# Optimization experiments

Measured on AMD Instinct MI355X. Metric: run time of the kernel, lower is better.

## Reference

```python
import jax, jax.numpy as jnp
import numpy as np

B, OBS, NH, LAT = 8192, 256, 2048, 128

def setup_inputs() -> dict:
    key = jax.random.key(0)
    k1, k2, k3, k4, k5, k6 = jax.random.split(key, 6)
    s1 = 1.0 / np.sqrt(OBS + NH)
    s2 = 1.0 / np.sqrt(NH)
    return {
        "x": jax.random.normal(k1, (B, OBS), dtype=jnp.float32),
        "h": jax.random.normal(k2, (B, NH), dtype=jnp.float32),
        "W_i2h": jax.random.normal(k3, (NH, OBS + NH), dtype=jnp.float32) * s1,
        "b_i2h": jax.random.normal(k4, (NH,), dtype=jnp.float32) * s1,
        "W_h2o": jax.random.normal(k5, (2 * LAT, NH), dtype=jnp.float32) * s2,
        "b_h2o": jax.random.normal(k6, (2 * LAT,), dtype=jnp.float32) * s2,
    }

def reference(x, h, W_i2h, b_i2h, W_h2o, b_h2o):
    # combined = cat((x, h), dim=1)  -> [B, OBS+NH]
    combined = jnp.concatenate([x, h], axis=1)
    # h_new = tanh(i2h(combined));  Linear is y = x @ W.T + b
    h_new = jnp.tanh(combined @ W_i2h.T + b_i2h)
    out = h_new @ W_h2o.T + b_h2o  # [B, 2*LAT]
    return (out, h_new)
```

## Files before the change

### kernel.cpp

```cpp
#include <hip/hip_runtime.h>
#include <hip/hip_bf16.h>
#include <cstdint>

using bf16 = __hip_bfloat16;
typedef __attribute__((ext_vector_type(8))) short short8;
typedef __attribute__((ext_vector_type(4))) float floatx4;

static constexpr int BATCH = 8192;
static constexpr int K1    = 2304;
static constexpr int N1    = 2048;
static constexpr int K2    = 2048;
static constexpr int N2    = 256;
static constexpr int KT1   = K1 / 64;

__device__ __forceinline__ void gload_lds16(const void* g, void* l) {
  __builtin_amdgcn_global_load_lds(
      (const __attribute__((address_space(1))) void*)g,
      (__attribute__((address_space(3))) void*)l, 16, 0, 0);
}

__device__ __forceinline__ float fast_tanh(float x) {
  float e = __builtin_amdgcn_exp2f(x * 2.8853900817779268f);
  return 1.0f - 2.0f * __builtin_amdgcn_rcpf(e + 1.0f);
}

__device__ __forceinline__ short8 cvt8(const float* src) {
  float4 a = ((const float4*)src)[0];
  float4 b = ((const float4*)src)[1];
  union { short8 v; bf16 e[8]; } u;
  u.e[0] = __float2bfloat16(a.x); u.e[1] = __float2bfloat16(a.y);
  u.e[2] = __float2bfloat16(a.z); u.e[3] = __float2bfloat16(a.w);
  u.e[4] = __float2bfloat16(b.x); u.e[5] = __float2bfloat16(b.y);
  u.e[6] = __float2bfloat16(b.z); u.e[7] = __float2bfloat16(b.w);
  return u.v;
}

static constexpr int SEG0 = BATCH * (K1 / 8);
static constexpr int SEG1 = N1 * K1 / 8;
static constexpr int SEG2 = N2 * K2 / 8;
__global__ __launch_bounds__(256) void prep(
    const float* __restrict__ x, const float* __restrict__ h,
    const float* __restrict__ W1, const float* __restrict__ W2,
    bf16* __restrict__ comb, bf16* __restrict__ W1b, bf16* __restrict__ W2b) {
  int i = blockIdx.x * 256 + threadIdx.x;
  if (i < SEG0) {
    int row  = i / 288;
    int slot = i - row * 288;
    const float* src = (slot < 32) ? (x + (size_t)row * 256 + slot * 8)
                                   : (h + (size_t)row * 2048 + (slot - 32) * 8);
    *(short8*)(comb + (size_t)row * 2304 + slot * 8) = cvt8(src);
  } else if (i < SEG0 + SEG1) {
    int j = i - SEG0;
    *(short8*)(W1b + (size_t)j * 8) = cvt8(W1 + (size_t)j * 8);
  } else {
    int j = i - (SEG0 + SEG1);
    *(short8*)(W2b + (size_t)j * 8) = cvt8(W2 + (size_t)j * 8);
  }
}

__global__ __launch_bounds__(256) void bias_init(
    const float* __restrict__ bias, float* __restrict__ out) {
  int i = blockIdx.x * 256 + threadIdx.x;
  float4 b = ((const float4*)bias)[i & 63];
  ((float4*)out)[i] = b;
}

__global__ __launch_bounds__(512, 2) void gemm1_tanh(
    const bf16* __restrict__ A, const bf16* __restrict__ W,
    const float* __restrict__ bias,
    float* __restrict__ hf32, bf16* __restrict__ hb16) {
  __shared__ bf16 lds[2][2][2][8192];
  const int t    = threadIdx.x;
  const int lane = t & 63;
  const int wave = t >> 6;
  const int wm   = (wave >> 2) * 128;
  const int wn   = (wave & 3) * 64;
  const int quad = lane >> 4;
  const int r15  = lane & 15;

  const int srow  = t >> 2;
  const int sslot = t & 3;
  const int sq    = (sslot ^ (srow & 3)) * 8;

  const size_t Abase = (size_t)blockIdx.x * 256 * K1;
  const size_t Bbase = (size_t)blockIdx.y * 256 * K1;
  const size_t gA0 = Abase + (size_t)srow * K1 + sq;
  const size_t gA1 = Abase + (size_t)(srow + 128) * K1 + sq;
  const size_t gB0 = Bbase + (size_t)srow * K1 + sq;
  const size_t gB1 = Bbase + (size_t)(srow + 128) * K1 + sq;
  const int d0 = t * 16, d1 = 8192 + t * 16;

#define STAGE(sb, mat_, skh, skt) do {                                       \
    const int ktc_ = ((skt) < KT1 ? (skt) : (KT1 - 1));                      \
    const size_t ko_ = (size_t)ktc_ * 64 + (skh) * 32;                       \
    const bf16* p0_ = (mat_) ? (W + gB0 + ko_) : (A + gA0 + ko_);            \
    const bf16* p1_ = (mat_) ? (W + gB1 + ko_) : (A + gA1 + ko_);            \
    gload_lds16(p0_, (char*)&lds[sb][mat_][skh][0] + d0);                    \
    gload_lds16(p1_, (char*)&lds[sb][mat_][skh][0] + d1);                    \
  } while (0)

  floatx4 acc[8][4];
  const floatx4 z = {0.f, 0.f, 0.f, 0.f};
#pragma unroll
  for (int i = 0; i < 8; i++)
#pragma unroll
    for (int j = 0; j < 4; j++) acc[i][j] = z;

  STAGE(0, 0, 0, 0); STAGE(0, 1, 0, 0); STAGE(0, 0, 1, 0); STAGE(0, 1, 1, 0);
  STAGE(1, 0, 0, 1); STAGE(1, 1, 0, 1);
  asm volatile("s_waitcnt vmcnt(4)" ::: "memory");
  __builtin_amdgcn_s_barrier();

#define PHASE(cb, ks, mtg, sb, smat, skh, skt, VMW) do {                     \
    short8 af_[4], bf_[4];                                                   \
    _Pragma("unroll")                                                        \
    for (int mt = 0; mt < 4; ++mt) {                                         \
      const int row = wm + (mtg) * 64 + mt * 16 + r15;                       \
      af_[mt] = *(const short8*)((const char*)&lds[cb][0][ks][0] +           \
                                 row * 64 + ((quad ^ (row & 3)) << 4));      \
    }                                                                        \
    _Pragma("unroll")                                                        \
    for (int nt = 0; nt < 4; ++nt) {                                         \
      const int row = wn + nt * 16 + r15;                                    \
      bf_[nt] = *(const short8*)((const char*)&lds[cb][1][ks][0] +           \
                                 row * 64 + ((quad ^ (row & 3)) << 4));      \
    }                                                                        \
    STAGE(sb, smat, skh, skt);                                               \
    __builtin_amdgcn_sched_barrier(0);                                       \
    if (VMW) asm volatile("s_waitcnt vmcnt(4)" ::: "memory");                \
    __builtin_amdgcn_s_barrier();                                            \
    asm volatile("s_waitcnt lgkmcnt(0)" ::: "memory");                       \
    __builtin_amdgcn_sched_barrier(0);                                       \
    __builtin_amdgcn_s_setprio(1);                                           \
    _Pragma("unroll")                                                        \
    for (int mt = 0; mt < 4; ++mt)                                           \
      _Pragma("unroll")                                                      \
      for (int nt = 0; nt < 4; ++nt)                                         \
        acc[(mtg) * 4 + mt][nt] = __builtin_amdgcn_mfma_f32_16x16x32_bf16(   \
            af_[mt], bf_[nt], acc[(mtg) * 4 + mt][nt], 0, 0, 0);             \
    __builtin_amdgcn_s_setprio(0);                                           \
    __builtin_amdgcn_s_barrier();                                            \
  } while (0)

#pragma clang loop unroll(disable)
  for (int t2 = 0; t2 < KT1 / 2; ++t2) {
    const int n = 2 * t2;
    PHASE(0, 0, 0,  1, 0, 1, n + 1, 0);
    PHASE(0, 0, 1,  1, 1, 1, n + 1, 0);
    PHASE(0, 1, 0,  0, 0, 0, n + 2, 0);
    PHASE(0, 1, 1,  0, 1, 0, n + 2, 1);
    PHASE(1, 0, 0,  0, 0, 1, n + 2, 0);
    PHASE(1, 0, 1,  0, 1, 1, n + 2, 0);
    PHASE(1, 1, 0,  1, 0, 0, n + 3, 0);
    PHASE(1, 1, 1,  1, 1, 0, n + 3, 1);
  }
#undef PHASE
#undef STAGE

  const int gcol0 = blockIdx.y * 256 + wn;
  float bv[4];
#pragma unroll
  for (int nt = 0; nt < 4; ++nt) bv[nt] = bias[gcol0 + nt * 16 + r15];
  const size_t grow0 = (size_t)blockIdx.x * 256 + wm;
#pragma unroll
  for (int mt = 0; mt < 8; ++mt) {
#pragma unroll
    for (int i = 0; i < 4; ++i) {
      const size_t gr = grow0 + mt * 16 + quad * 4 + i;
      const size_t rb = gr * (size_t)N1;
#pragma unroll
      for (int nt = 0; nt < 4; ++nt) {
        const int gc = gcol0 + nt * 16 + r15;
        float v = fast_tanh(acc[mt][nt][i] + bv[nt]);
        hf32[rb + gc] = v;
        hb16[rb + gc] = __float2bfloat16(v);
      }
    }
  }
}

__global__ __launch_bounds__(256) void gemm2_out(
    const bf16* __restrict__ A, const bf16* __restrict__ W,
    float* __restrict__ out) {
  __shared__ bf16 As[32 * 64];
  __shared__ bf16 Bs[256 * 64];
  const int t    = threadIdx.x;
  const int lane = t & 63;
  const int wave = t >> 6;
  const int quad = lane >> 4;
  const int r15  = lane & 15;
  const int srow = t >> 3;
  const int sc   = t & 7;

  const int mrow0 = blockIdx.x * 32;
  const int kbase = blockIdx.y * (K2 / 2);

  floatx4 acc[2][4];
  const floatx4 z = {0.f, 0.f, 0.f, 0.f};
#pragma unroll
  for (int i = 0; i < 2; i++)
#pragma unroll
    for (int j = 0; j < 4; j++) acc[i][j] = z;

  for (int kt = 0; kt < 16; ++kt) {
    const int k0 = kbase + kt * 64;
    __syncthreads();
    {
      int row = srow;
      int gc  = k0 + ((sc ^ (row & 7)) << 3);
      gload_lds16(A + (size_t)(mrow0 + row) * K2 + gc, (char*)As + t * 16);
    }
#pragma unroll
    for (int it = 0; it < 8; ++it) {
      int row = it * 32 + srow;
      int gc  = k0 + ((sc ^ (row & 7)) << 3);
      gload_lds16(W + (size_t)row * K2 + gc,
                  (char*)Bs + it * 4096 + t * 16);
    }
    __syncthreads();
#pragma unroll
    for (int ks = 0; ks < 2; ++ks) {
      short8 af[2], bfr[4];
      const int kq = ks * 4 + quad;
#pragma unroll
      for (int mt = 0; mt < 2; ++mt) {
        int row = mt * 16 + r15;
        af[mt] = *(const short8*)((const char*)As + row * 128 +
                                  ((kq ^ (row & 7)) << 4));
      }
#pragma unroll
      for (int nt = 0; nt < 4; ++nt) {
        int row = wave * 64 + nt * 16 + r15;
        bfr[nt] = *(const short8*)((const char*)Bs + row * 128 +
                                   ((kq ^ (row & 7)) << 4));
      }
#pragma unroll
      for (int mt = 0; mt < 2; ++mt)
#pragma unroll
        for (int nt = 0; nt < 4; ++nt)
          acc[mt][nt] = __builtin_amdgcn_mfma_f32_16x16x32_bf16(
              af[mt], bfr[nt], acc[mt][nt], 0, 0, 0);
    }
  }

  const int gcol0 = wave * 64;
#pragma unroll
  for (int mt = 0; mt < 2; ++mt) {
#pragma unroll
    for (int i = 0; i < 4; ++i) {
      size_t gr = (size_t)mrow0 + mt * 16 + quad * 4 + i;
      size_t rb = gr * (size_t)N2;
#pragma unroll
      for (int nt = 0; nt < 4; ++nt) {
        int gc = gcol0 + nt * 16 + r15;
        unsafeAtomicAdd(&out[rb + gc], acc[mt][nt][i]);
      }
    }
  }
}

extern "C" void kernel_launch(void* const* d_in, const int* in_sizes, int n_in,
                              void* d_out, int out_size, void* d_ws,
                              size_t ws_size, hipStream_t stream) {
  const float* x     = (const float*)d_in[0];
  const float* h     = (const float*)d_in[1];
  const float* W_i2h = (const float*)d_in[2];
  const float* b_i2h = (const float*)d_in[3];
  const float* W_h2o = (const float*)d_in[4];
  const float* b_h2o = (const float*)d_in[5];

  float* out       = (float*)d_out;
  float* hnew_f32  = out + (size_t)BATCH * N2;

  bf16* comb   = (bf16*)d_ws;
  bf16* Wi2h_b = comb + (size_t)BATCH * K1;
  bf16* Wh2o_b = Wi2h_b + (size_t)N1 * K1;
  bf16* hnew_b = Wh2o_b + (size_t)N2 * K2;

  bias_init<<<(BATCH * N2 / 4) / 256, 256, 0, stream>>>(b_h2o, out);

  prep<<<(SEG0 + SEG1 + SEG2) / 256, 256, 0, stream>>>(
      x, h, W_i2h, W_h2o, comb, Wi2h_b, Wh2o_b);

  gemm1_tanh<<<dim3(BATCH / 256, N1 / 256), 512, 0, stream>>>(
      comb, Wi2h_b, b_i2h, hnew_f32, hnew_b);

  gemm2_out<<<dim3(BATCH / 32, 2), 256, 0, stream>>>(hnew_b, Wh2o_b, out);
}
```

Before: 266.7 us.

## Merge bias init into prep, restructure gemm1 phases, double-buffer gemm2

```diff
diff --git a/kernel.cpp b/kernel.cpp
--- a/kernel.cpp
+++ b/kernel.cpp
@@ -38,10 +38,13 @@
 static constexpr int SEG0 = BATCH * (K1 / 8);
 static constexpr int SEG1 = N1 * K1 / 8;
 static constexpr int SEG2 = N2 * K2 / 8;
+static constexpr int SEG3 = BATCH * (N2 / 4);
 __global__ __launch_bounds__(256) void prep(
     const float* __restrict__ x, const float* __restrict__ h,
     const float* __restrict__ W1, const float* __restrict__ W2,
-    bf16* __restrict__ comb, bf16* __restrict__ W1b, bf16* __restrict__ W2b) {
+    const float* __restrict__ b2,
+    bf16* __restrict__ comb, bf16* __restrict__ W1b, bf16* __restrict__ W2b,
+    float* __restrict__ outp) {
   int i = blockIdx.x * 256 + threadIdx.x;
   if (i < SEG0) {
     int row  = i / 288;
@@ -52,17 +55,14 @@
   } else if (i < SEG0 + SEG1) {
     int j = i - SEG0;
     *(short8*)(W1b + (size_t)j * 8) = cvt8(W1 + (size_t)j * 8);
-  } else {
+  } else if (i < SEG0 + SEG1 + SEG2) {
     int j = i - (SEG0 + SEG1);
     *(short8*)(W2b + (size_t)j * 8) = cvt8(W2 + (size_t)j * 8);
-  }
-}
-
-__global__ __launch_bounds__(256) void bias_init(
-    const float* __restrict__ bias, float* __restrict__ out) {
-  int i = blockIdx.x * 256 + threadIdx.x;
-  float4 b = ((const float4*)bias)[i & 63];
-  ((float4*)out)[i] = b;
+  } else {
+    int j = i - (SEG0 + SEG1 + SEG2);
+    float4 b = ((const float4*)b2)[j & 63];
+    ((float4*)outp)[j] = b;
+  }
 }
 
 __global__ __launch_bounds__(512, 2) void gemm1_tanh(
@@ -78,9 +78,13 @@
   const int quad = lane >> 4;
   const int r15  = lane & 15;
 
+  const int swz   = ((quad ^ ((r15 >> 1) & 3)) << 4);
+  const int baseA = wm * 64 + r15 * 64 + swz;
+  const int baseB = 32768 + wn * 64 + r15 * 64 + swz;
+
   const int srow  = t >> 2;
   const int sslot = t & 3;
-  const int sq    = (sslot ^ (srow & 3)) * 8;
+  const int sq    = (sslot ^ ((srow >> 1) & 3)) * 8;
 
   const size_t Abase = (size_t)blockIdx.x * 256 * K1;
   const size_t Bbase = (size_t)blockIdx.y * 256 * K1;
@@ -89,14 +93,16 @@
   const size_t gB0 = Bbase + (size_t)srow * K1 + sq;
   const size_t gB1 = Bbase + (size_t)(srow + 128) * K1 + sq;
   const int d0 = t * 16, d1 = 8192 + t * 16;
-
-#define STAGE(sb, mat_, skh, skt) do {                                       \
+  char* const ldsb = (char*)lds;
+
+#define STAGE2(sb, skh, skt) do {                                            \
     const int ktc_ = ((skt) < KT1 ? (skt) : (KT1 - 1));                      \
     const size_t ko_ = (size_t)ktc_ * 64 + (skh) * 32;                       \
-    const bf16* p0_ = (mat_) ? (W + gB0 + ko_) : (A + gA0 + ko_);            \
-    const bf16* p1_ = (mat_) ? (W + gB1 + ko_) : (A + gA1 + ko_);            \
-    gload_lds16(p0_, (char*)&lds[sb][mat_][skh][0] + d0);                    \
-    gload_lds16(p1_, (char*)&lds[sb][mat_][skh][0] + d1);                    \
+    char* const la_ = ldsb + ((sb) << 16) + ((skh) << 14);                   \
+    gload_lds16(A + gA0 + ko_, la_ + d0);                                    \
+    gload_lds16(A + gA1 + ko_, la_ + d1);                                    \
+    gload_lds16(W + gB0 + ko_, la_ + 32768 + d0);                            \
+    gload_lds16(W + gB1 + ko_, la_ + 32768 + d1);                            \
   } while (0)
 
   floatx4 acc[8][4];
@@ -106,38 +112,48 @@
 #pragma unroll
     for (int j = 0; j < 4; j++) acc[i][j] = z;
 
-  STAGE(0, 0, 0, 0); STAGE(0, 1, 0, 0); STAGE(0, 0, 1, 0); STAGE(0, 1, 1, 0);
-  STAGE(1, 0, 0, 1); STAGE(1, 1, 0, 1);
+  STAGE2(0, 0, 0); STAGE2(0, 1, 0); STAGE2(1, 0, 1);
   asm volatile("s_waitcnt vmcnt(4)" ::: "memory");
   __builtin_amdgcn_s_barrier();
 
-#define PHASE(cb, ks, mtg, sb, smat, skh, skt, VMW) do {                     \
-    short8 af_[4], bf_[4];                                                   \
-    _Pragma("unroll")                                                        \
-    for (int mt = 0; mt < 4; ++mt) {                                         \
-      const int row = wm + (mtg) * 64 + mt * 16 + r15;                       \
-      af_[mt] = *(const short8*)((const char*)&lds[cb][0][ks][0] +           \
-                                 row * 64 + ((quad ^ (row & 3)) << 4));      \
-    }                                                                        \
-    _Pragma("unroll")                                                        \
-    for (int nt = 0; nt < 4; ++nt) {                                         \
-      const int row = wn + nt * 16 + r15;                                    \
-      bf_[nt] = *(const short8*)((const char*)&lds[cb][1][ks][0] +           \
-                                 row * 64 + ((quad ^ (row & 3)) << 4));      \
-    }                                                                        \
-    STAGE(sb, smat, skh, skt);                                               \
-    __builtin_amdgcn_sched_barrier(0);                                       \
-    if (VMW) asm volatile("s_waitcnt vmcnt(4)" ::: "memory");                \
+#define MPHASE(cb, ks, sb, skh, skt, VMW) do {                               \
+    STAGE2(sb, skh, skt);                                                    \
+    __builtin_amdgcn_sched_barrier(0);                                       \
+    if (VMW) asm volatile("s_waitcnt vmcnt(8)" ::: "memory");                \
     __builtin_amdgcn_s_barrier();                                            \
-    asm volatile("s_waitcnt lgkmcnt(0)" ::: "memory");                       \
+    asm volatile("" ::: "memory");          \
+    const char* Lb_ = ldsb + ((cb) << 16) + ((ks) << 14);                    \
+    short8 bf_[4], af0_[4], af1_[4];                                         \
+    _Pragma("unroll")                                                        \
+    for (int nt = 0; nt < 4; ++nt)                                           \
+      bf_[nt] = *(const short8*)(Lb_ + baseB + nt * 1024);                   \
+    _Pragma("unroll")                                                        \
+    for (int mt = 0; mt < 4; ++mt)                                           \
+      af0_[mt] = *(const short8*)(Lb_ + baseA + mt * 1024);                  \
+    __builtin_amdgcn_sched_barrier(0);                                       \
+    _Pragma("unroll")                                                        \
+    for (int mt = 0; mt < 4; ++mt)                                           \
+      af1_[mt] = *(const short8*)(Lb_ + baseA + 4096 + mt * 1024);           \
+    __builtin_amdgcn_sched_barrier(0);                                       \
+    asm volatile("s_waitcnt lgkmcnt(4)" ::: "memory");                       \
     __builtin_amdgcn_sched_barrier(0);                                       \
     __builtin_amdgcn_s_setprio(1);                                           \
     _Pragma("unroll")                                                        \
     for (int mt = 0; mt < 4; ++mt)                                           \
       _Pragma("unroll")                                                      \
       for (int nt = 0; nt < 4; ++nt)                                         \
-        acc[(mtg) * 4 + mt][nt] = __builtin_amdgcn_mfma_f32_16x16x32_bf16(   \
-            af_[mt], bf_[nt], acc[(mtg) * 4 + mt][nt], 0, 0, 0);             \
+        acc[mt][nt] = __builtin_amdgcn_mfma_f32_16x16x32_bf16(               \
+            af0_[mt], bf_[nt], acc[mt][nt], 0, 0, 0);                        \
+    __builtin_amdgcn_s_setprio(0);                                           \
+    asm volatile("s_waitcnt lgkmcnt(0)" ::: "memory");                       \
+    __builtin_amdgcn_sched_barrier(0);                                       \
+    __builtin_amdgcn_s_setprio(1);                                           \
+    _Pragma("unroll")                                                        \
+    for (int mt = 0; mt < 4; ++mt)                                           \
+      _Pragma("unroll")                                                      \
+      for (int nt = 0; nt < 4; ++nt)                                         \
+        acc[4 + mt][nt] = __builtin_amdgcn_mfma_f32_16x16x32_bf16(           \
+            af1_[mt], bf_[nt], acc[4 + mt][nt], 0, 0, 0);                    \
     __builtin_amdgcn_s_setprio(0);                                           \
     __builtin_amdgcn_s_barrier();                                            \
   } while (0)
@@ -145,17 +161,13 @@
 #pragma clang loop unroll(disable)
   for (int t2 = 0; t2 < KT1 / 2; ++t2) {
     const int n = 2 * t2;
-    PHASE(0, 0, 0,  1, 0, 1, n + 1, 0);
-    PHASE(0, 0, 1,  1, 1, 1, n + 1, 0);
-    PHASE(0, 1, 0,  0, 0, 0, n + 2, 0);
-    PHASE(0, 1, 1,  0, 1, 0, n + 2, 1);
-    PHASE(1, 0, 0,  0, 0, 1, n + 2, 0);
-    PHASE(1, 0, 1,  0, 1, 1, n + 2, 0);
-    PHASE(1, 1, 0,  1, 0, 0, n + 3, 0);
-    PHASE(1, 1, 1,  1, 1, 0, n + 3, 1);
-  }
-#undef PHASE
-#undef STAGE
+    MPHASE(0, 0,  1, 1, n + 1, 0);
+    MPHASE(0, 1,  0, 0, n + 2, 1);
+    MPHASE(1, 0,  0, 1, n + 2, 0);
+    MPHASE(1, 1,  1, 0, n + 3, 1);
+  }
+#undef MPHASE
+#undef STAGE2
 
   const int gcol0 = blockIdx.y * 256 + wn;
   float bv[4];
@@ -182,8 +194,8 @@
 __global__ __launch_bounds__(256) void gemm2_out(
     const bf16* __restrict__ A, const bf16* __restrict__ W,
     float* __restrict__ out) {
-  __shared__ bf16 As[32 * 64];
-  __shared__ bf16 Bs[256 * 64];
+  __shared__ bf16 As[2][32 * 64];
+  __shared__ bf16 Bs[2][256 * 64];
   const int t    = threadIdx.x;
   const int lane = t & 63;
   const int wave = t >> 6;
@@ -195,6 +207,22 @@
   const int mrow0 = blockIdx.x * 32;
   const int kbase = blockIdx.y * (K2 / 2);
 
+#define G2STAGE(b, kt) do {                                                  \
+    const int k0_ = kbase + (kt) * 64;                                       \
+    {                                                                        \
+      int gc_ = k0_ + ((sc ^ (srow & 7)) << 3);                              \
+      gload_lds16(A + (size_t)(mrow0 + srow) * K2 + gc_,                     \
+                  (char*)As[b] + t * 16);                                    \
+    }                                                                        \
+    _Pragma("unroll")                                                        \
+    for (int it = 0; it < 8; ++it) {                                         \
+      int row_ = it * 32 + srow;                                             \
+      int gc_  = k0_ + ((sc ^ (row_ & 7)) << 3);                             \
+      gload_lds16(W + (size_t)row_ * K2 + gc_,                               \
+                  (char*)Bs[b] + it * 4096 + t * 16);                        \
+    }                                                                        \
+  } while (0)
+
   floatx4 acc[2][4];
   const floatx4 z = {0.f, 0.f, 0.f, 0.f};
 #pragma unroll
@@ -202,22 +230,18 @@
 #pragma unroll
     for (int j = 0; j < 4; j++) acc[i][j] = z;
 
+  G2STAGE(0, 0);
+#pragma clang loop unroll(disable)
   for (int kt = 0; kt < 16; ++kt) {
-    const int k0 = kbase + kt * 64;
-    __syncthreads();
-    {
-      int row = srow;
-      int gc  = k0 + ((sc ^ (row & 7)) << 3);
-      gload_lds16(A + (size_t)(mrow0 + row) * K2 + gc, (char*)As + t * 16);
+    const int cur = kt & 1;
+    if (kt + 1 < 16) {
+      G2STAGE(cur ^ 1, kt + 1);
+      asm volatile("s_waitcnt vmcnt(9)" ::: "memory");
+    } else {
+      asm volatile("s_waitcnt vmcnt(0)" ::: "memory");
     }
-#pragma unroll
-    for (int it = 0; it < 8; ++it) {
-      int row = it * 32 + srow;
-      int gc  = k0 + ((sc ^ (row & 7)) << 3);
-      gload_lds16(W + (size_t)row * K2 + gc,
-                  (char*)Bs + it * 4096 + t * 16);
-    }
-    __syncthreads();
+    __builtin_amdgcn_s_barrier();
+    asm volatile("" ::: "memory");
 #pragma unroll
     for (int ks = 0; ks < 2; ++ks) {
       short8 af[2], bfr[4];
@@ -225,13 +249,13 @@
 #pragma unroll
       for (int mt = 0; mt < 2; ++mt) {
         int row = mt * 16 + r15;
-        af[mt] = *(const short8*)((const char*)As + row * 128 +
+        af[mt] = *(const short8*)((const char*)As[cur] + row * 128 +
                                   ((kq ^ (row & 7)) << 4));
       }
 #pragma unroll
       for (int nt = 0; nt < 4; ++nt) {
         int row = wave * 64 + nt * 16 + r15;
-        bfr[nt] = *(const short8*)((const char*)Bs + row * 128 +
+        bfr[nt] = *(const short8*)((const char*)Bs[cur] + row * 128 +
                                    ((kq ^ (row & 7)) << 4));
       }
 #pragma unroll
@@ -241,7 +265,10 @@
           acc[mt][nt] = __builtin_amdgcn_mfma_f32_16x16x32_bf16(
               af[mt], bfr[nt], acc[mt][nt], 0, 0, 0);
     }
-  }
+    asm volatile("" ::: "memory");
+    __builtin_amdgcn_s_barrier();
+  }
+#undef G2STAGE
 
   const int gcol0 = wave * 64;
 #pragma unroll
@@ -277,10 +304,8 @@
   bf16* Wh2o_b = Wi2h_b + (size_t)N1 * K1;
   bf16* hnew_b = Wh2o_b + (size_t)N2 * K2;
 
-  bias_init<<<(BATCH * N2 / 4) / 256, 256, 0, stream>>>(b_h2o, out);
-
-  prep<<<(SEG0 + SEG1 + SEG2) / 256, 256, 0, stream>>>(
-      x, h, W_i2h, W_h2o, comb, Wi2h_b, Wh2o_b);
+  prep<<<(SEG0 + SEG1 + SEG2 + SEG3) / 256, 256, 0, stream>>>(
+      x, h, W_i2h, W_h2o, b_h2o, comb, Wi2h_b, Wh2o_b, out);
 
   gemm1_tanh<<<dim3(BATCH / 256, N1 / 256), 512, 0, stream>>>(
       comb, Wi2h_b, b_i2h, hnew_f32, hnew_b);
```

After: 260.2 us. 2.4% less time.
